# Performance work log

Hardware: AMD Instinct MI355X
Metric: run time of the kernel (lower is better)

## Reference

```python
import jax, jax.numpy as jnp
import numpy as np

N = 100000   # nodes
E = 800000   # edges
G = 512      # graphs in batch
F_IN = 75    # num_features_xd


def setup_inputs() -> dict:
    key = jax.random.key(0)
    ks = jax.random.split(key, 12)
    s = 0.05
    x = jax.random.normal(ks[0], (N, F_IN), jnp.float32)
    edge_index = jax.random.randint(ks[1], (2, E), 0, N, dtype=jnp.int32)
    # deterministic near-equal graph assignment (sorted, no empty graphs)
    batch = ((jnp.arange(N) * G) // N).astype(jnp.int32)
    W1 = jax.random.normal(ks[2], (F_IN, F_IN), jnp.float32) * s
    b1 = jnp.zeros((F_IN,), jnp.float32)
    W2 = jax.random.normal(ks[3], (F_IN, 2 * F_IN), jnp.float32) * s
    b2 = jnp.zeros((2 * F_IN,), jnp.float32)
    W3 = jax.random.normal(ks[4], (2 * F_IN, 4 * F_IN), jnp.float32) * s
    b3 = jnp.zeros((4 * F_IN,), jnp.float32)
    Wg1 = jax.random.normal(ks[5], (4 * F_IN, 1024), jnp.float32) * s
    bg1 = jnp.zeros((1024,), jnp.float32)
    Wg2 = jax.random.normal(ks[6], (1024, 128), jnp.float32) * s
    bg2 = jnp.zeros((128,), jnp.float32)
    return {"x": x, "edge_index": edge_index, "batch": batch,
            "W1": W1, "b1": b1, "W2": W2, "b2": b2, "W3": W3, "b3": b3,
            "Wg1": Wg1, "bg1": bg1, "Wg2": Wg2, "bg2": bg2}


def reference(x, edge_index, batch, W1, b1, W2, b2, W3, b3, Wg1, bg1, Wg2, bg2):
    n = x.shape[0]
    row, col = edge_index[0], edge_index[1]
    loop = jnp.arange(n, dtype=row.dtype)
    row_f = jnp.concatenate([row, loop])  # source (with self loops)
    col_f = jnp.concatenate([col, loop])  # target
    # symmetric GCN normalization: deg from targets incl. self loops
    deg = jax.ops.segment_sum(jnp.ones_like(col_f, dtype=x.dtype), col_f, num_segments=n)
    dinv = jnp.where(deg > 0, deg ** -0.5, 0.0)
    norm = dinv[row_f] * dinv[col_f]  # [E+N]

    def gcn(h, W, b):
        h = h @ W  # transform first (PyG GCNConv order)
        msg = norm[:, None] * h[row_f]  # gather + scale
        return jax.ops.segment_sum(msg, col_f, num_segments=n) + b

    h = jax.nn.relu(gcn(x, W1, b1))
    h = jax.nn.relu(gcn(h, W2, b2))
    h = jax.nn.relu(gcn(h, W3, b3))
    g = jax.ops.segment_max(h, batch, num_segments=G)  # global max pool -> [G, 300]
    g = jax.nn.relu(g @ Wg1 + bg1)
    # dropout is identity at inference
    return g @ Wg2 + bg2  # [G, 128]
```

## Files before the change

kernel.cpp:

```cpp
#include <hip/hip_runtime.h>

typedef __attribute__((ext_vector_type(8))) short short8v;
typedef __attribute__((ext_vector_type(4))) float f32x4;
typedef unsigned short u16;

__device__ inline u16 f2bf(float x){
  union{float f; unsigned u;} v; v.f = x;
  unsigned r = (v.u + 0x7FFFu + ((v.u >> 16) & 1u)) >> 16;
  return (u16)r;
}
__device__ inline float b2f(u16 u){
  union{unsigned u32; float f;} w; w.u32 = (unsigned)u << 16; return w.f;
}


__global__ void k_deg(const int* __restrict__ col, int* __restrict__ indeg, int E){
  int e = blockIdx.x*blockDim.x + threadIdx.x;
  if (e < E) atomicAdd(&indeg[col[e]], 1);
}

__global__ void k_dinv(const int* __restrict__ indeg, float* __restrict__ dinv, int n){
  int i = blockIdx.x*blockDim.x + threadIdx.x;
  if (i < n) dinv[i] = rsqrtf((float)(indeg[i] + 1));
}

__global__ __launch_bounds__(256) void k_scan1(const int* __restrict__ indeg, int* __restrict__ rp,
                                               int* __restrict__ bsums, int n){
  __shared__ int s[256];
  int b = blockIdx.x, t = threadIdx.x;
  int base = b*1024 + t*4;
  int v[4]; int tsum = 0;
  #pragma unroll
  for (int j=0;j<4;j++){ v[j] = (base+j < n) ? indeg[base+j] : 0; tsum += v[j]; }
  s[t] = tsum; __syncthreads();
  for (int d=1; d<256; d<<=1){ int x = (t>=d) ? s[t-d] : 0; __syncthreads(); s[t] += x; __syncthreads(); }
  int run = s[t] - tsum;
  if (t == 255) bsums[b] = s[255];
  #pragma unroll
  for (int j=0;j<4;j++){ if (base+j < n){ rp[base+j] = run; } run += v[j]; }
}

__global__ __launch_bounds__(128) void k_scan2(int* bsums, int* rp, int nb, int n){
  __shared__ int s[128];
  int t = threadIdx.x;
  int orig = (t < nb) ? bsums[t] : 0;
  s[t] = orig; __syncthreads();
  for (int d=1; d<128; d<<=1){ int x = (t>=d) ? s[t-d] : 0; __syncthreads(); s[t] += x; __syncthreads(); }
  if (t < nb) bsums[t] = s[t] - orig;
  if (t == 127) rp[n] = s[127];
}

__global__ void k_scan3(int* __restrict__ rp, int* __restrict__ nxt, const int* __restrict__ bsums, int n){
  int i = blockIdx.x*blockDim.x + threadIdx.x;
  if (i < n){ int v = rp[i] + bsums[i >> 10]; rp[i] = v; nxt[i] = v; }
}

__global__ void k_scatter(const int* __restrict__ row, const int* __restrict__ col,
                          int* __restrict__ nxt, int* __restrict__ csr, int E){
  int e = blockIdx.x*blockDim.x + threadIdx.x;
  if (e < E){ int c = col[e]; int p = atomicAdd(&nxt[c], 1); csr[p] = row[e]; }
}

__global__ void k_padb(const float* __restrict__ x, u16* __restrict__ xb, int n){
  long total = (long)n*80;
  for (long idx = blockIdx.x*(long)blockDim.x + threadIdx.x; idx < total; idx += (long)gridDim.x*blockDim.x){
    int r = (int)(idx/80), fcol = (int)(idx%80);
    xb[idx] = f2bf(fcol < 75 ? x[(size_t)r*75 + fcol] : 0.f);
  }
}

__global__ void k_wt(const float* __restrict__ W, u16* __restrict__ Wt,
                     int Kreal, int NC, int KPAD, int NCP){
  int idx = blockIdx.x*blockDim.x + threadIdx.x;
  if (idx >= NCP*KPAD) return;
  int c = idx / KPAD, k = idx % KPAD;
  float v = (c < NC && k < Kreal) ? W[(size_t)k*NC + c] : 0.0f;
  Wt[idx] = f2bf(v);
}


template<int FP>
__global__ __launch_bounds__(256) void k_prop_bf(const u16* __restrict__ h, const float* __restrict__ dinv,
                                                 const int* __restrict__ rp, const int* __restrict__ csr,
                                                 u16* __restrict__ out, int n){
  constexpr int TPN = FP/8;
  constexpr int NPB = 256/TPN;
  int q = threadIdx.x / TPN;
  int t = threadIdx.x - q*TPN;
  if (q >= NPB) return;
  int node = blockIdx.x*NPB + q;
  if (node >= n) return;
  int f = 8*t;
  float di = dinv[node];
  float acc[8];
  {
    short8v v = *(const short8v*)&h[(size_t)node*FP + f];
    #pragma unroll
    for (int i=0;i<8;i++) acc[i] = di*b2f((u16)v[i]);
  }
  int e0 = rp[node], e1 = rp[node+1];
  int e = e0;
  for (; e + 4 <= e1; e += 4){
    int s0 = csr[e], s1 = csr[e+1], s2 = csr[e+2], s3 = csr[e+3];
    float d0 = dinv[s0], d1 = dinv[s1], d2 = dinv[s2], d3 = dinv[s3];
    short8v v0 = *(const short8v*)&h[(size_t)s0*FP + f];
    short8v v1 = *(const short8v*)&h[(size_t)s1*FP + f];
    short8v v2 = *(const short8v*)&h[(size_t)s2*FP + f];
    short8v v3 = *(const short8v*)&h[(size_t)s3*FP + f];
    #pragma unroll
    for (int i=0;i<8;i++)
      acc[i] += d0*b2f((u16)v0[i]) + d1*b2f((u16)v1[i]) + d2*b2f((u16)v2[i]) + d3*b2f((u16)v3[i]);
  }
  for (; e < e1; ++e){
    int s = csr[e]; float ds = dinv[s];
    short8v v = *(const short8v*)&h[(size_t)s*FP + f];
    #pragma unroll
    for (int i=0;i<8;i++) acc[i] += ds*b2f((u16)v[i]);
  }
  short8v o;
  #pragma unroll
  for (int i=0;i<8;i++) o[i] = (short)f2bf(di*acc[i]);
  *(short8v*)&out[(size_t)node*FP + f] = o;
}


template<int KPAD, int LDA, int POOL>
__global__ __launch_bounds__(256) void k_gemm_bf(
    const u16* __restrict__ A, const u16* __restrict__ Wt,
    const float* __restrict__ bias,
    u16* __restrict__ out, int ldout, int NC, int NT,
    const int* __restrict__ batch, unsigned* __restrict__ gpool, int ldg,
    int n, int G)
{
  constexpr int SA = KPAD + 8;
  constexpr int SW = KPAD + 8;
  constexpr int C8 = KPAD/8;
  constexpr int R8 = LDA/8;
  __shared__ u16 As[64*SA];
  __shared__ u16 Ws[64*SW];
  __shared__ unsigned pmax[2][64];

  int tid = threadIdx.x;
  int r0 = blockIdx.x * 64;
  int w = tid >> 6, l = tid & 63;

  #pragma unroll
  for (int i = 0; i < 64*C8/256; ++i){
    int idx = tid + 256*i;
    int r = idx / C8, c8 = idx % C8;
    short8v v = (short8v){0,0,0,0,0,0,0,0};
    if (r0 + r < n && c8 < R8) v = *(const short8v*)&A[(size_t)(r0+r)*LDA + 8*c8];
    *(short8v*)&As[r*SA + 8*c8] = v;
  }

  const u16* Ab = &As[(16*w + (l & 15))*SA + (l >> 4)*8];
  const u16* Bb = &Ws[(l & 15)*SW + (l >> 4)*8];

  for (int ct = 0; ct < NT; ++ct){
    if (ct) __syncthreads();
    #pragma unroll
    for (int i = 0; i < 64*C8/256; ++i){
      int idx = tid + 256*i;
      int wr = idx / C8, wk = idx % C8;
      *(short8v*)&Ws[wr*SW + 8*wk] = *(const short8v*)&Wt[(size_t)(ct*64 + wr)*KPAD + 8*wk];
    }
    if (POOL){ if (tid < 128) pmax[tid>>6][tid&63] = 0u; }
    __syncthreads();

    f32x4 acc[4];
    #pragma unroll
    for (int b=0;b<4;b++) acc[b] = (f32x4){0.f,0.f,0.f,0.f};

    #pragma unroll
    for (int ks = 0; ks < KPAD/32; ++ks){
      short8v a0 = *(const short8v*)(Ab + ks*32);
      short8v b0 = *(const short8v*)(Bb + ks*32);
      short8v b1 = *(const short8v*)(Bb + 16*SW + ks*32);
      short8v b2 = *(const short8v*)(Bb + 32*SW + ks*32);
      short8v b3 = *(const short8v*)(Bb + 48*SW + ks*32);
      acc[0] = __builtin_amdgcn_mfma_f32_16x16x32_bf16(a0, b0, acc[0], 0, 0, 0);
      acc[1] = __builtin_amdgcn_mfma_f32_16x16x32_bf16(a0, b1, acc[1], 0, 0, 0);
      acc[2] = __builtin_amdgcn_mfma_f32_16x16x32_bf16(a0, b2, acc[2], 0, 0, 0);
      acc[3] = __builtin_amdgcn_mfma_f32_16x16x32_bf16(a0, b3, acc[3], 0, 0, 0);
    }

    int rbase = r0 + 16*w + 4*(l >> 4);
    int cbase = ct*64;
    if (!POOL){
      #pragma unroll
      for (int cf=0;cf<4;cf++){
        int c = cbase + 16*cf + (l & 15);
        if (c >= ldout) continue;
        bool real = (c < NC);
        float bv = real ? bias[c] : 0.f;
        #pragma unroll
        for (int r=0;r<4;r++){
          int rr = rbase + r;
          if (rr < n){
            float v = real ? fmaxf(acc[cf][r] + bv, 0.f) : 0.f;
            out[(size_t)rr*ldout + c] = f2bf(v);
          }
        }
      }
    } else {
      int g0 = batch[r0];
      #pragma unroll
      for (int cf=0;cf<4;cf++){
        int c = cbase + 16*cf + (l & 15);
        if (c >= NC) continue;
        float bv = bias[c];
        int curgi = -1; float m = 0.f;
        #pragma unroll
        for (int r=0;r<4;r++){
          int rr = rbase + r;
          if (rr < n){
            int gi = batch[rr] - g0; if (gi > 1) gi = 1;
            float v = fmaxf(acc[cf][r] + bv, 0.f);
            if (gi != curgi){
              if (curgi >= 0 && m > 0.f) atomicMax(&pmax[curgi][16*cf + (l&15)], __float_as_uint(m));
              curgi = gi; m = v;
            } else m = fmaxf(m, v);
          }
        }
        if (curgi >= 0 && m > 0.f) atomicMax(&pmax[curgi][16*cf + (l&15)], __float_as_uint(m));
      }
      __syncthreads();
      if (tid < 128){
        int gi = tid >> 6, cc = tid & 63;
        unsigned v = pmax[gi][cc];
        int gg = g0 + gi;
        if (v != 0u && (cbase + cc) < NC && gg < G)
          atomicMax(&gpool[(size_t)gg*ldg + (cbase + cc)], v);
      }
    }
  }
}


__global__ __launch_bounds__(256) void k_gemm_kloop(
    const float* __restrict__ A, int lda, int Ktot,
    const u16* __restrict__ Wt, int ldw,
    const float* __restrict__ bias,
    float* __restrict__ out, int ldout, int NC,
    int n, int relu)
{
  constexpr int SA = 72, SW = 72;
  __shared__ u16 As[128*SA];
  __shared__ u16 Ws[64*SW];
  int tid = threadIdx.x;
  int r0 = blockIdx.x * 128, c0 = blockIdx.y * 64;
  int w = tid >> 6, l = tid & 63;

  f32x4 acc[2][4];
  #pragma unroll
  for (int a=0;a<2;a++)
    #pragma unroll
    for (int b=0;b<4;b++) acc[a][b] = (f32x4){0.f,0.f,0.f,0.f};

  const u16* Ab = &As[(32*w + (l & 15))*SA + (l >> 4)*8];
  const u16* Bb = &Ws[(l & 15)*SW + (l >> 4)*8];

  for (int k0 = 0; k0 < Ktot; k0 += 64){
    #pragma unroll
    for (int i=0;i<8;i++){
      int idx = tid + 256*i;
      int r = idx >> 4, c4 = idx & 15;
      float4 v = make_float4(0.f,0.f,0.f,0.f);
      if (r0 + r < n) v = *(const float4*)&A[(size_t)(r0+r)*lda + k0 + 4*c4];
      unsigned p01 = (unsigned)f2bf(v.x) | ((unsigned)f2bf(v.y) << 16);
      unsigned p23 = (unsigned)f2bf(v.z) | ((unsigned)f2bf(v.w) << 16);
      *(uint2*)&As[r*SA + 4*c4] = make_uint2(p01, p23);
    }
    #pragma unroll
    for (int i=0;i<2;i++){
      int idx = tid + 256*i;
      int wr = idx >> 3, wk = idx & 7;
      short8v wv = *(const short8v*)&Wt[(size_t)(c0+wr)*ldw + k0 + 8*wk];
      *(short8v*)&Ws[wr*SW + 8*wk] = wv;
    }
    __syncthreads();
    #pragma unroll
    for (int ks = 0; ks < 2; ++ks){
      short8v a0 = *(const short8v*)(Ab + ks*32);
      short8v a1 = *(const short8v*)(Ab + 16*SA + ks*32);
      short8v b0 = *(const short8v*)(Bb + ks*32);
      short8v b1 = *(const short8v*)(Bb + 16*SW + ks*32);
      short8v b2 = *(const short8v*)(Bb + 32*SW + ks*32);
      short8v b3 = *(const short8v*)(Bb + 48*SW + ks*32);
      acc[0][0] = __builtin_amdgcn_mfma_f32_16x16x32_bf16(a0, b0, acc[0][0], 0, 0, 0);
      acc[0][1] = __builtin_amdgcn_mfma_f32_16x16x32_bf16(a0, b1, acc[0][1], 0, 0, 0);
      acc[0][2] = __builtin_amdgcn_mfma_f32_16x16x32_bf16(a0, b2, acc[0][2], 0, 0, 0);
      acc[0][3] = __builtin_amdgcn_mfma_f32_16x16x32_bf16(a0, b3, acc[0][3], 0, 0, 0);
      acc[1][0] = __builtin_amdgcn_mfma_f32_16x16x32_bf16(a1, b0, acc[1][0], 0, 0, 0);
      acc[1][1] = __builtin_amdgcn_mfma_f32_16x16x32_bf16(a1, b1, acc[1][1], 0, 0, 0);
      acc[1][2] = __builtin_amdgcn_mfma_f32_16x16x32_bf16(a1, b2, acc[1][2], 0, 0, 0);
      acc[1][3] = __builtin_amdgcn_mfma_f32_16x16x32_bf16(a1, b3, acc[1][3], 0, 0, 0);
    }
    __syncthreads();
  }

  #pragma unroll
  for (int rf=0;rf<2;rf++){
    int rbase = r0 + 32*w + 16*rf + 4*(l >> 4);
    #pragma unroll
    for (int cf=0;cf<4;cf++){
      int c = c0 + 16*cf + (l & 15);
      if (c >= NC) continue;
      float bv = bias[c];
      #pragma unroll
      for (int r=0;r<4;r++){
        int rr = rbase + r;
        if (rr < n){
          float v = acc[rf][cf][r] + bv;
          if (relu) v = fmaxf(v, 0.f);
          out[(size_t)rr*ldout + c] = v;
        }
      }
    }
  }
}


extern "C" void kernel_launch(void* const* d_in, const int* in_sizes, int n_in,
                              void* d_out, int out_size, void* d_ws, size_t ws_size,
                              hipStream_t stream)
{
  const float* x   = (const float*)d_in[0];
  const int*   ei  = (const int*)d_in[1];
  const int*   batch = (const int*)d_in[2];
  const float* W1  = (const float*)d_in[3]; const float* b1  = (const float*)d_in[4];
  const float* W2  = (const float*)d_in[5]; const float* b2  = (const float*)d_in[6];
  const float* W3  = (const float*)d_in[7]; const float* b3  = (const float*)d_in[8];
  const float* Wg1 = (const float*)d_in[9]; const float* bg1 = (const float*)d_in[10];
  const float* Wg2 = (const float*)d_in[11]; const float* bg2 = (const float*)d_in[12];
  float* out = (float*)d_out;

  const int F1 = 75;
  int n = in_sizes[0] / F1;
  int E = in_sizes[1] / 2;
  int G = out_size / 128;
  const int* row = ei;
  const int* col = ei + E;

  char* ws = (char*)d_ws;
  size_t off = 0;
  auto alloc = [&](size_t bytes){ size_t o = off; off += (bytes + 255) & ~(size_t)255; return o; };
  u16*   xb    = (u16*)  (ws + alloc((size_t)n*80*2));
  u16*   qb    = (u16*)  (ws + alloc((size_t)n*160*2));
  u16*   h2b   = (u16*)  (ws + alloc((size_t)n*160*2));
  float* dinv  = (float*)(ws + alloc((size_t)n*4));
  int*   indeg = (int*)  (ws + alloc((size_t)n*4));
  int*   rp    = (int*)  (ws + alloc((size_t)(n+1)*4));
  int*   nxt   = (int*)  (ws + alloc((size_t)n*4));
  int*   csr   = (int*)  (ws + alloc((size_t)E*4));
  int*   bsums = (int*)  (ws + alloc(1024*4));
  unsigned* g  = (unsigned*)(ws + alloc((size_t)G*320*4));
  float* gh    = (float*)(ws + alloc((size_t)G*1024*4));
  u16* Wt1  = (u16*)(ws + alloc((size_t)128*96*2));
  u16* Wt2  = (u16*)(ws + alloc((size_t)192*96*2));
  u16* Wt3  = (u16*)(ws + alloc((size_t)320*160*2));
  u16* Wg1t = (u16*)(ws + alloc((size_t)1024*320*2));
  u16* Wg2t = (u16*)(ws + alloc((size_t)128*1024*2));
  u16* h1b = xb;

  hipMemsetAsync(indeg, 0, (size_t)n*4, stream);
  hipMemsetAsync(g, 0, (size_t)G*320*4, stream);

  k_deg<<<(E+255)/256, 256, 0, stream>>>(col, indeg, E);
  k_dinv<<<(n+255)/256, 256, 0, stream>>>(indeg, dinv, n);

  int nb = (n + 1023) / 1024;
  k_scan1<<<nb, 256, 0, stream>>>(indeg, rp, bsums, n);
  k_scan2<<<1, 128, 0, stream>>>(bsums, rp, nb, n);
  k_scan3<<<(n+255)/256, 256, 0, stream>>>(rp, nxt, bsums, n);
  k_scatter<<<(E+255)/256, 256, 0, stream>>>(row, col, nxt, csr, E);

  k_padb<<<4096, 256, 0, stream>>>(x, xb, n);
  k_wt<<<(128*96+255)/256, 256, 0, stream>>>(W1, Wt1, 75, 75, 96, 128);
  k_wt<<<(192*96+255)/256, 256, 0, stream>>>(W2, Wt2, 75, 150, 96, 192);
  k_wt<<<(320*160+255)/256, 256, 0, stream>>>(W3, Wt3, 150, 300, 160, 320);
  k_wt<<<(1024*320+255)/256, 256, 0, stream>>>(Wg1, Wg1t, 300, 1024, 320, 1024);
  k_wt<<<(128*1024+255)/256, 256, 0, stream>>>(Wg2, Wg2t, 1024, 128, 1024, 128);

  int mb64 = (n + 63) / 64;

  k_prop_bf<80><<<(n+24)/25, 256, 0, stream>>>(xb, dinv, rp, csr, qb, n);
  k_gemm_bf<96,80,0><<<mb64, 256, 0, stream>>>(qb, Wt1, b1, h1b, 80, 75, 2,
                                               nullptr, nullptr, 0, n, G);
  k_prop_bf<80><<<(n+24)/25, 256, 0, stream>>>(h1b, dinv, rp, csr, qb, n);
  k_gemm_bf<96,80,0><<<mb64, 256, 0, stream>>>(qb, Wt2, b2, h2b, 160, 150, 3,
                                               nullptr, nullptr, 0, n, G);
  k_prop_bf<160><<<(n+11)/12, 256, 0, stream>>>(h2b, dinv, rp, csr, qb, n);
  k_gemm_bf<160,160,1><<<mb64, 256, 0, stream>>>(qb, Wt3, b3, nullptr, 0, 300, 5,
                                                 batch, g, 320, n, G);
  {
    dim3 grid(G/128, 1024/64);
    k_gemm_kloop<<<grid, 256, 0, stream>>>((const float*)g, 320, 320, Wg1t, 320, bg1,
                                           gh, 1024, 1024, G, 1);
  }
  {
    dim3 grid(G/128, 128/64);
    k_gemm_kloop<<<grid, 256, 0, stream>>>(gh, 1024, 1024, Wg2t, 1024, bg2,
                                           out, 128, 128, G, 0);
  }
}
```

Measured before the change: 494.5 us.

## Split-K the head GEMMs with a reduce kernel and prefetch weight tiles in registers

The two small head GEMMs (512 rows) used to launch very few blocks, each looping over K serially. They now split K across blockIdx.z into per-chunk partial sums, and a separate reduce kernel adds the bias and applies ReLU. This raises the block count at the price of extra partial-buffer traffic and two more launches. The node GEMM also prefetches the next column tile of weights into registers before the MFMA loop, overlapping global loads with compute at the cost of extra registers.

```diff
diff --git a/kernel.cpp b/kernel.cpp
--- a/kernel.cpp
+++ b/kernel.cpp
@@ -136,6 +136,7 @@
   constexpr int SW = KPAD + 8;
   constexpr int C8 = KPAD/8;
   constexpr int R8 = LDA/8;
+  constexpr int WL = 64*C8/256;
   __shared__ u16 As[64*SA];
   __shared__ u16 Ws[64*SW];
   __shared__ unsigned pmax[2][64];
@@ -153,19 +154,36 @@
     *(short8v*)&As[r*SA + 8*c8] = v;
   }
 
+  short8v wreg[WL];
+  #pragma unroll
+  for (int i = 0; i < WL; ++i){
+    int idx = tid + 256*i;
+    int wr = idx / C8, wk = idx % C8;
+    wreg[i] = *(const short8v*)&Wt[(size_t)wr*KPAD + 8*wk];
+  }
+
   const u16* Ab = &As[(16*w + (l & 15))*SA + (l >> 4)*8];
   const u16* Bb = &Ws[(l & 15)*SW + (l >> 4)*8];
 
   for (int ct = 0; ct < NT; ++ct){
-    if (ct) __syncthreads();
-    #pragma unroll
-    for (int i = 0; i < 64*C8/256; ++i){
+    __syncthreads();
+    #pragma unroll
+    for (int i = 0; i < WL; ++i){
       int idx = tid + 256*i;
       int wr = idx / C8, wk = idx % C8;
-      *(short8v*)&Ws[wr*SW + 8*wk] = *(const short8v*)&Wt[(size_t)(ct*64 + wr)*KPAD + 8*wk];
+      *(short8v*)&Ws[wr*SW + 8*wk] = wreg[i];
     }
     if (POOL){ if (tid < 128) pmax[tid>>6][tid&63] = 0u; }
     __syncthreads();
+
+    if (ct + 1 < NT){
+      #pragma unroll
+      for (int i = 0; i < WL; ++i){
+        int idx = tid + 256*i;
+        int wr = idx / C8, wk = idx % C8;
+        wreg[i] = *(const short8v*)&Wt[(size_t)((ct+1)*64 + wr)*KPAD + 8*wk];
+      }
+    }
 
     f32x4 acc[4];
     #pragma unroll
@@ -237,68 +255,65 @@
 }
 
 
-__global__ __launch_bounds__(256) void k_gemm_kloop(
-    const float* __restrict__ A, int lda, int Ktot,
+__global__ __launch_bounds__(256) void k_gemm_kc(
+    const float* __restrict__ A, int lda,
     const u16* __restrict__ Wt, int ldw,
-    const float* __restrict__ bias,
-    float* __restrict__ out, int ldout, int NC,
-    int n, int relu)
+    float* __restrict__ P, int ldp,
+    int rows, int NC)
 {
   constexpr int SA = 72, SW = 72;
   __shared__ u16 As[128*SA];
   __shared__ u16 Ws[64*SW];
   int tid = threadIdx.x;
-  int r0 = blockIdx.x * 128, c0 = blockIdx.y * 64;
+  int r0 = blockIdx.x * 128, c0 = blockIdx.y * 64, k0 = blockIdx.z * 64;
   int w = tid >> 6, l = tid & 63;
 
-  f32x4 acc[2][4];
-  #pragma unroll
-  for (int a=0;a<2;a++)
-    #pragma unroll
-    for (int b=0;b<4;b++) acc[a][b] = (f32x4){0.f,0.f,0.f,0.f};
+  #pragma unroll
+  for (int i=0;i<8;i++){
+    int idx = tid + 256*i;
+    int r = idx >> 4, c4 = idx & 15;
+    float4 v = make_float4(0.f,0.f,0.f,0.f);
+    if (r0 + r < rows) v = *(const float4*)&A[(size_t)(r0+r)*lda + k0 + 4*c4];
+    unsigned p01 = (unsigned)f2bf(v.x) | ((unsigned)f2bf(v.y) << 16);
+    unsigned p23 = (unsigned)f2bf(v.z) | ((unsigned)f2bf(v.w) << 16);
+    *(uint2*)&As[r*SA + 4*c4] = make_uint2(p01, p23);
+  }
+  #pragma unroll
+  for (int i=0;i<2;i++){
+    int idx = tid + 256*i;
+    int wr = idx >> 3, wk = idx & 7;
+    *(short8v*)&Ws[wr*SW + 8*wk] = *(const short8v*)&Wt[(size_t)(c0+wr)*ldw + k0 + 8*wk];
+  }
+  __syncthreads();
 
   const u16* Ab = &As[(32*w + (l & 15))*SA + (l >> 4)*8];
   const u16* Bb = &Ws[(l & 15)*SW + (l >> 4)*8];
 
-  for (int k0 = 0; k0 < Ktot; k0 += 64){
-    #pragma unroll
-    for (int i=0;i<8;i++){
-      int idx = tid + 256*i;
-      int r = idx >> 4, c4 = idx & 15;
-      float4 v = make_float4(0.f,0.f,0.f,0.f);
-      if (r0 + r < n) v = *(const float4*)&A[(size_t)(r0+r)*lda + k0 + 4*c4];
-      unsigned p01 = (unsigned)f2bf(v.x) | ((unsigned)f2bf(v.y) << 16);
-      unsigned p23 = (unsigned)f2bf(v.z) | ((unsigned)f2bf(v.w) << 16);
-      *(uint2*)&As[r*SA + 4*c4] = make_uint2(p01, p23);
-    }
-    #pragma unroll
-    for (int i=0;i<2;i++){
-      int idx = tid + 256*i;
-      int wr = idx >> 3, wk = idx & 7;
-      short8v wv = *(const short8v*)&Wt[(size_t)(c0+wr)*ldw + k0 + 8*wk];
-      *(short8v*)&Ws[wr*SW + 8*wk] = wv;
-    }
-    __syncthreads();
-    #pragma unroll
-    for (int ks = 0; ks < 2; ++ks){
-      short8v a0 = *(const short8v*)(Ab + ks*32);
-      short8v a1 = *(const short8v*)(Ab + 16*SA + ks*32);
-      short8v b0 = *(const short8v*)(Bb + ks*32);
-      short8v b1 = *(const short8v*)(Bb + 16*SW + ks*32);
-      short8v b2 = *(const short8v*)(Bb + 32*SW + ks*32);
-      short8v b3 = *(const short8v*)(Bb + 48*SW + ks*32);
-      acc[0][0] = __builtin_amdgcn_mfma_f32_16x16x32_bf16(a0, b0, acc[0][0], 0, 0, 0);
-      acc[0][1] = __builtin_amdgcn_mfma_f32_16x16x32_bf16(a0, b1, acc[0][1], 0, 0, 0);
-      acc[0][2] = __builtin_amdgcn_mfma_f32_16x16x32_bf16(a0, b2, acc[0][2], 0, 0, 0);
-      acc[0][3] = __builtin_amdgcn_mfma_f32_16x16x32_bf16(a0, b3, acc[0][3], 0, 0, 0);
-      acc[1][0] = __builtin_amdgcn_mfma_f32_16x16x32_bf16(a1, b0, acc[1][0], 0, 0, 0);
-      acc[1][1] = __builtin_amdgcn_mfma_f32_16x16x32_bf16(a1, b1, acc[1][1], 0, 0, 0);
-      acc[1][2] = __builtin_amdgcn_mfma_f32_16x16x32_bf16(a1, b2, acc[1][2], 0, 0, 0);
-      acc[1][3] = __builtin_amdgcn_mfma_f32_16x16x32_bf16(a1, b3, acc[1][3], 0, 0, 0);
-    }
-    __syncthreads();
-  }
-
+  f32x4 acc[2][4];
+  #pragma unroll
+  for (int a=0;a<2;a++)
+    #pragma unroll
+    for (int b=0;b<4;b++) acc[a][b] = (f32x4){0.f,0.f,0.f,0.f};
+
+  #pragma unroll
+  for (int ks = 0; ks < 2; ++ks){
+    short8v a0 = *(const short8v*)(Ab + ks*32);
+    short8v a1 = *(const short8v*)(Ab + 16*SA + ks*32);
+    short8v b0 = *(const short8v*)(Bb + ks*32);
+    short8v b1 = *(const short8v*)(Bb + 16*SW + ks*32);
+    short8v b2 = *(const short8v*)(Bb + 32*SW + ks*32);
+    short8v b3 = *(const short8v*)(Bb + 48*SW + ks*32);
+    acc[0][0] = __builtin_amdgcn_mfma_f32_16x16x32_bf16(a0, b0, acc[0][0], 0, 0, 0);
+    acc[0][1] = __builtin_amdgcn_mfma_f32_16x16x32_bf16(a0, b1, acc[0][1], 0, 0, 0);
+    acc[0][2] = __builtin_amdgcn_mfma_f32_16x16x32_bf16(a0, b2, acc[0][2], 0, 0, 0);
+    acc[0][3] = __builtin_amdgcn_mfma_f32_16x16x32_bf16(a0, b3, acc[0][3], 0, 0, 0);
+    acc[1][0] = __builtin_amdgcn_mfma_f32_16x16x32_bf16(a1, b0, acc[1][0], 0, 0, 0);
+    acc[1][1] = __builtin_amdgcn_mfma_f32_16x16x32_bf16(a1, b1, acc[1][1], 0, 0, 0);
+    acc[1][2] = __builtin_amdgcn_mfma_f32_16x16x32_bf16(a1, b2, acc[1][2], 0, 0, 0);
+    acc[1][3] = __builtin_amdgcn_mfma_f32_16x16x32_bf16(a1, b3, acc[1][3], 0, 0, 0);
+  }
+
+  float* Pk = P + (size_t)blockIdx.z * rows * ldp;
   #pragma unroll
   for (int rf=0;rf<2;rf++){
     int rbase = r0 + 32*w + 16*rf + 4*(l >> 4);
@@ -306,18 +321,33 @@
     for (int cf=0;cf<4;cf++){
       int c = c0 + 16*cf + (l & 15);
       if (c >= NC) continue;
-      float bv = bias[c];
       #pragma unroll
       for (int r=0;r<4;r++){
         int rr = rbase + r;
-        if (rr < n){
-          float v = acc[rf][cf][r] + bv;
-          if (relu) v = fmaxf(v, 0.f);
-          out[(size_t)rr*ldout + c] = v;
-        }
+        if (rr < rows) Pk[(size_t)rr*ldp + c] = acc[rf][cf][r];
       }
     }
   }
+}
+
+__global__ __launch_bounds__(256) void k_reduce(
+    const float* __restrict__ P, int nk, int rows, int NC,
+    const float* __restrict__ bias, float* __restrict__ out, int relu)
+{
+  int i = blockIdx.x*blockDim.x + threadIdx.x;
+  int tot = rows*(NC/4);
+  if (i >= tot) return;
+  int r = i / (NC/4), c4 = i % (NC/4);
+  float4 acc = *(const float4*)&bias[4*c4];
+  for (int kc = 0; kc < nk; ++kc){
+    float4 p = *(const float4*)&P[((size_t)kc*rows + r)*NC + 4*c4];
+    acc.x += p.x; acc.y += p.y; acc.z += p.z; acc.w += p.w;
+  }
+  if (relu){
+    acc.x = fmaxf(acc.x, 0.f); acc.y = fmaxf(acc.y, 0.f);
+    acc.z = fmaxf(acc.z, 0.f); acc.w = fmaxf(acc.w, 0.f);
+  }
+  *(float4*)&out[(size_t)r*NC + 4*c4] = acc;
 }
 
 
@@ -356,6 +386,8 @@
   int*   bsums = (int*)  (ws + alloc(1024*4));
   unsigned* g  = (unsigned*)(ws + alloc((size_t)G*320*4));
   float* gh    = (float*)(ws + alloc((size_t)G*1024*4));
+  float* ph1   = (float*)(ws + alloc((size_t)5*G*1024*4));
+  float* ph2   = (float*)(ws + alloc((size_t)16*G*128*4));
   u16* Wt1  = (u16*)(ws + alloc((size_t)128*96*2));
   u16* Wt2  = (u16*)(ws + alloc((size_t)192*96*2));
   u16* Wt3  = (u16*)(ws + alloc((size_t)320*160*2));
@@ -394,13 +426,15 @@
   k_gemm_bf<160,160,1><<<mb64, 256, 0, stream>>>(qb, Wt3, b3, nullptr, 0, 300, 5,
                                                  batch, g, 320, n, G);
   {
-    dim3 grid(G/128, 1024/64);
-    k_gemm_kloop<<<grid, 256, 0, stream>>>((const float*)g, 320, 320, Wg1t, 320, bg1,
-                                           gh, 1024, 1024, G, 1);
+    dim3 grid((G+127)/128, 1024/64, 5);
+    k_gemm_kc<<<grid, 256, 0, stream>>>((const float*)g, 320, Wg1t, 320, ph1, 1024, G, 1024);
+    int tot = G*(1024/4);
+    k_reduce<<<(tot+255)/256, 256, 0, stream>>>(ph1, 5, G, 1024, bg1, gh, 1);
   }
   {
-    dim3 grid(G/128, 128/64);
-    k_gemm_kloop<<<grid, 256, 0, stream>>>(gh, 1024, 1024, Wg2t, 1024, bg2,
-                                           out, 128, 128, G, 0);
-  }
-}
+    dim3 grid((G+127)/128, 128/64, 16);
+    k_gemm_kc<<<grid, 256, 0, stream>>>(gh, 1024, Wg2t, 1024, ph2, 128, G, 128);
+    int tot = G*(128/4);
+    k_reduce<<<(tot+255)/256, 256, 0, stream>>>(ph2, 16, G, 128, bg2, out, 0);
+  }
+}
```

Measured after the change: 434.9 us. 1.14x faster.
